# Optimization experiments

Hardware: AMD Instinct MI355X
Metric: run time of the kernel (lower is better)

Reference implementation:

```python
import jax, jax.numpy as jnp
import numpy as np
import math

B, S, D, H = 4, 1024, 1024, 16
DK = D // H
WINDOW = 128
NEG = -100000.0


def setup_inputs() -> dict:
    key = jax.random.key(0)
    kx, kw1, kb1, kw2, kb2 = jax.random.split(key, 5)
    x = jax.random.normal(kx, (B, S, D), dtype=jnp.float32)
    # sliding-window band mask: True where |i-j| <= WINDOW
    i = jnp.arange(S)
    band = (jnp.abs(i[:, None] - i[None, :]) <= WINDOW)
    mask = jnp.broadcast_to(band, (B, S, S))
    # second structured mask: causal
    causal = (i[:, None] >= i[None, :])
    mask2 = jnp.broadcast_to(causal, (B, S, S))
    scale = 1.0 / math.sqrt(D)
    Wqkv = jax.random.normal(kw1, (D, 3 * D), dtype=jnp.float32) * scale
    bqkv = jax.random.normal(kb1, (3 * D,), dtype=jnp.float32) * 0.01
    Wo = jax.random.normal(kw2, (D, D), dtype=jnp.float32) * scale
    bo = jax.random.normal(kb2, (D,), dtype=jnp.float32) * 0.01
    return {"x": x, "mask": mask, "mask2": mask2, "Wqkv": Wqkv, "bqkv": bqkv, "Wo": Wo, "bo": bo}


def reference(x, mask, mask2, Wqkv, bqkv, Wo, bo):
    b, s, d = x.shape
    qkv = x @ Wqkv + bqkv                      # [b, s, 3d]
    q, k, v = jnp.split(qkv, 3, axis=-1)
    # [b, s, h, dk] -> [b, h, s, dk]
    q = q.reshape(b, s, H, DK).transpose(0, 2, 1, 3)
    k = k.reshape(b, s, H, DK).transpose(0, 2, 1, 3)
    v = v.reshape(b, s, H, DK).transpose(0, 2, 1, 3)
    scores = jnp.einsum('bhtd,bhsd->bhts', q, k) / math.sqrt(DK)
    scores = jnp.where(mask[:, None, :, :], scores, NEG)
    scores = jnp.where(mask2[:, None, :, :], scores, NEG)
    weights = jax.nn.softmax(scores, axis=-1)  # [b, h, t, s]
    context = jnp.einsum('bhts,bhsd->bhtd', weights, v)
    context = context.transpose(0, 2, 1, 3).reshape(b, s, d)
    context = context @ Wo + bo
    return (context, weights)
```

## Files before the change

### kernel.cpp

```cpp
#include <hip/hip_runtime.h>

typedef short bf16x8 __attribute__((ext_vector_type(8)));
typedef float floatx4 __attribute__((ext_vector_type(4)));

#define GLOBAL_AS __attribute__((address_space(1)))
#define LDS_AS __attribute__((address_space(3)))

__device__ __forceinline__ void gload_lds16(const ushort* g, ushort* l) {
  __builtin_amdgcn_global_load_lds((const GLOBAL_AS void*)g, (LDS_AS void*)l, 16, 0, 0);
}

__device__ __forceinline__ ushort f2bf(float x) {
  uint u = __float_as_uint(x);
  return (ushort)((u + 0x7fffu + ((u >> 16) & 1u)) >> 16);
}

__global__ __launch_bounds__(256) void k_f32_to_bf16(const float4* __restrict__ in,
                                                     ushort4* __restrict__ out, int n4) {
  int g = blockIdx.x * 256 + threadIdx.x;
  if (g < n4) {
    float4 v = in[g];
    ushort4 o;
    o.x = f2bf(v.x); o.y = f2bf(v.y); o.z = f2bf(v.z); o.w = f2bf(v.w);
    out[g] = o;
  }
}

__global__ __launch_bounds__(256) void k_transpose2(const float* __restrict__ W1,
                                                    ushort* __restrict__ O1,
                                                    const float* __restrict__ W2,
                                                    ushort* __restrict__ O2) {
  __shared__ float tile[32][33];
  int bx = blockIdx.x;
  const float* in; ushort* out; int N;
  if (bx < 96) { in = W1; out = O1; N = 3072; }
  else         { in = W2; out = O2; N = 1024; bx -= 96; }
  const int K = 1024;
  int n0 = bx * 32, k0 = blockIdx.y * 32;
  int tx = threadIdx.x & 31, ty = threadIdx.x >> 5;
  #pragma unroll
  for (int r = ty; r < 32; r += 8)
    tile[r][tx] = in[(size_t)(k0 + r) * N + n0 + tx];
  __syncthreads();
  #pragma unroll
  for (int r = ty; r < 32; r += 8)
    out[(size_t)(n0 + r) * K + k0 + tx] = f2bf(tile[tx][r]);
}

template <int OUT_BF16, int BN>
__global__ __launch_bounds__(256) void k_gemm_bt(const ushort* __restrict__ A,
                                                 const ushort* __restrict__ Bt,
                                                 const float* __restrict__ bias,
                                                 void* __restrict__ Cout,
                                                 int M, int N, int K) {
  constexpr int NI = BN / 32;
  constexpr int NB = BN / 64;
  __shared__ ushort As[128 * 32];
  __shared__ ushort Bs[BN * 32];
  const int t = threadIdx.x;
  const int m0 = blockIdx.y * 128, n0 = blockIdx.x * BN;
  const int w = t >> 6, l = t & 63;
  const int wm = (w & 1) * 64, wn = (w >> 1) * (BN / 2);
  const int lr = l & 15, q8 = (l >> 4) * 8;
  const int lrow = l >> 2, lcol = (l & 3) * 8;

  floatx4 acc[4][NI];
  #pragma unroll
  for (int i = 0; i < 4; ++i)
    #pragma unroll
    for (int j = 0; j < NI; ++j) acc[i][j] = (floatx4){0.f, 0.f, 0.f, 0.f};

  for (int k0 = 0; k0 < K; k0 += 32) {
    __syncthreads();
    #pragma unroll
    for (int i = 0; i < 2; ++i) {
      int r0 = (w * 2 + i) * 16;
      gload_lds16(A + (size_t)(m0 + r0 + lrow) * K + k0 + lcol, As + r0 * 32);
    }
    #pragma unroll
    for (int i = 0; i < NB; ++i) {
      int r0 = (w * NB + i) * 16;
      gload_lds16(Bt + (size_t)(n0 + r0 + lrow) * K + k0 + lcol, Bs + r0 * 32);
    }
    __syncthreads();
    bf16x8 af[4], bfr[NI];
    #pragma unroll
    for (int mi = 0; mi < 4; ++mi)
      af[mi] = *(const bf16x8*)(As + (wm + mi * 16 + lr) * 32 + q8);
    #pragma unroll
    for (int ni = 0; ni < NI; ++ni)
      bfr[ni] = *(const bf16x8*)(Bs + (wn + ni * 16 + lr) * 32 + q8);
    #pragma unroll
    for (int mi = 0; mi < 4; ++mi)
      #pragma unroll
      for (int ni = 0; ni < NI; ++ni)
        acc[mi][ni] = __builtin_amdgcn_mfma_f32_16x16x32_bf16(af[mi], bfr[ni], acc[mi][ni], 0, 0, 0);
  }

  const int rq = (l >> 4) * 4;
  #pragma unroll
  for (int ni = 0; ni < NI; ++ni) {
    int col = n0 + wn + ni * 16 + lr;
    float bv = bias[col];
    #pragma unroll
    for (int mi = 0; mi < 4; ++mi) {
      int row = m0 + wm + mi * 16 + rq;
      #pragma unroll
      for (int r2 = 0; r2 < 4; ++r2) {
        float v = acc[mi][ni][r2] + bv;
        size_t idx = (size_t)(row + r2) * N + col;
        if (OUT_BF16) ((ushort*)Cout)[idx] = f2bf(v);
        else          ((float*)Cout)[idx] = v;
      }
    }
  }
}

__global__ __launch_bounds__(256) void k_attn(const ushort* __restrict__ qkv,
                                              float* __restrict__ wout,
                                              ushort* __restrict__ ctxout) {
  __shared__ ushort smKP[192 * 68];
  __shared__ ushort smVT[64 * 200];
  __shared__ float smInv[64];

  const int t = threadIdx.x;
  const int w = t >> 6, l = t & 63;
  const int lr = l & 15, q8 = (l >> 4) * 8, q4 = (l >> 4) * 4;
  const int iblk = blockIdx.x & 15;
  const int h = (blockIdx.x >> 4) & 15;
  const int b = blockIdx.x >> 8;
  const int i0 = iblk * 64;
  const int jb0 = i0 - 128;
  const int tok0 = b * 1024 + i0;
  const int qoff = h * 64, koff = 1024 + h * 64, voff = 2048 + h * 64;
  const size_t wbase = ((size_t)(b * 16 + h) * 1024 + i0) * 1024;

  #pragma unroll
  for (int c = 0; c < 6; ++c) {
    int idx = t + 256 * c, row = idx >> 3, ch = idx & 7;
    int jsrc = jb0 + row; if (jsrc < 0) jsrc = 0;
    *(uint4*)(smKP + row * 68 + ch * 8) =
        *(const uint4*)(qkv + (size_t)(b * 1024 + jsrc) * 3072 + koff + ch * 8);
  }
  #pragma unroll
  for (int c = 0; c < 6; ++c) {
    int idx = t + 256 * c;
    int j = (idx & 15) + 16 * (idx >> 7);
    int d0 = ((idx >> 4) & 7) * 8;
    int jsrc = jb0 + j; if (jsrc < 0) jsrc = 0;
    uint4 u = *(const uint4*)(qkv + (size_t)(b * 1024 + jsrc) * 3072 + voff + d0);
    ushort* p = smVT + j;
    p[(d0 + 0) * 200] = (ushort)(u.x & 0xffffu);
    p[(d0 + 1) * 200] = (ushort)(u.x >> 16);
    p[(d0 + 2) * 200] = (ushort)(u.y & 0xffffu);
    p[(d0 + 3) * 200] = (ushort)(u.y >> 16);
    p[(d0 + 4) * 200] = (ushort)(u.z & 0xffffu);
    p[(d0 + 5) * 200] = (ushort)(u.z >> 16);
    p[(d0 + 6) * 200] = (ushort)(u.w & 0xffffu);
    p[(d0 + 7) * 200] = (ushort)(u.w >> 16);
  }

  const ushort* qrow = qkv + (size_t)(tok0 + w * 16 + lr) * 3072 + qoff;
  bf16x8 aq0 = *(const bf16x8*)(qrow + q8);
  bf16x8 aq1 = *(const bf16x8*)(qrow + 32 + q8);
  __syncthreads();

  floatx4 sc[12];
  #pragma unroll
  for (int ni = 0; ni < 12; ++ni) sc[ni] = (floatx4){0.f, 0.f, 0.f, 0.f};
  #pragma unroll
  for (int ni = 0; ni < 12; ++ni) {
    bf16x8 bk0 = *(const bf16x8*)(smKP + (ni * 16 + lr) * 68 + q8);
    bf16x8 bk1 = *(const bf16x8*)(smKP + (ni * 16 + lr) * 68 + 32 + q8);
    sc[ni] = __builtin_amdgcn_mfma_f32_16x16x32_bf16(aq0, bk0, sc[ni], 0, 0, 0);
    sc[ni] = __builtin_amdgcn_mfma_f32_16x16x32_bf16(aq1, bk1, sc[ni], 0, 0, 0);
  }
  __syncthreads();

  float mrow[4] = {-3e38f, -3e38f, -3e38f, -3e38f};
  #pragma unroll
  for (int ni = 0; ni < 12; ++ni) {
    int nj = ni * 16 + lr;
    #pragma unroll
    for (int reg = 0; reg < 4; ++reg) {
      int di = w * 16 + q4 + reg;
      bool valid = (nj >= di) & (nj <= di + 128) & (jb0 + nj >= 0);
      float s = valid ? sc[ni][reg] * 0.125f : -3e38f;
      sc[ni][reg] = s;
      mrow[reg] = fmaxf(mrow[reg], s);
    }
  }
  #pragma unroll
  for (int reg = 0; reg < 4; ++reg) {
    #pragma unroll
    for (int off = 1; off < 16; off <<= 1)
      mrow[reg] = fmaxf(mrow[reg], __shfl_xor(mrow[reg], off, 64));
  }
  float lrow[4] = {0.f, 0.f, 0.f, 0.f};
  #pragma unroll
  for (int ni = 0; ni < 12; ++ni) {
    #pragma unroll
    for (int reg = 0; reg < 4; ++reg) {
      float e = __expf(sc[ni][reg] - mrow[reg]);
      sc[ni][reg] = e;
      lrow[reg] += e;
    }
  }
  float inv[4];
  #pragma unroll
  for (int reg = 0; reg < 4; ++reg) {
    float s = lrow[reg];
    #pragma unroll
    for (int off = 1; off < 16; off <<= 1) s += __shfl_xor(s, off, 64);
    inv[reg] = 1.0f / s;
  }

  ushort* smP = smKP;
  #pragma unroll
  for (int ni = 0; ni < 12; ++ni) {
    int nj = ni * 16 + lr;
    #pragma unroll
    for (int reg = 0; reg < 4; ++reg) {
      int il = w * 16 + q4 + reg;
      smP[il * 204 + nj] = f2bf(sc[ni][reg]);
    }
  }
  if (lr == 0) {
    #pragma unroll
    for (int reg = 0; reg < 4; ++reg) smInv[w * 16 + q4 + reg] = inv[reg];
  }

  floatx4 oc[4];
  #pragma unroll
  for (int ni = 0; ni < 4; ++ni) oc[ni] = (floatx4){0.f, 0.f, 0.f, 0.f};
  #pragma unroll
  for (int ks = 0; ks < 6; ++ks) {
    bf16x8 ap = *(const bf16x8*)(smP + (w * 16 + lr) * 204 + ks * 32 + q8);
    #pragma unroll
    for (int ni = 0; ni < 4; ++ni) {
      bf16x8 bv = *(const bf16x8*)(smVT + (ni * 16 + lr) * 200 + ks * 32 + q8);
      oc[ni] = __builtin_amdgcn_mfma_f32_16x16x32_bf16(ap, bv, oc[ni], 0, 0, 0);
    }
  }

  #pragma unroll
  for (int ni = 0; ni < 4; ++ni) {
    int d = ni * 16 + lr;
    #pragma unroll
    for (int reg = 0; reg < 4; ++reg) {
      int il = w * 16 + q4 + reg;
      ctxout[(size_t)(tok0 + il) * 1024 + qoff + d] = f2bf(oc[ni][reg] * inv[reg]);
    }
  }

  __syncthreads();

  {
    const int j4 = t * 4;
    const unsigned nj4 = (unsigned)(j4 - jb0);
    const bool inband = nj4 < 192u;
    const int njc = inband ? (int)nj4 : 0;
    const float bandf = inband ? 1.0f : 0.0f;
    float* wp = wout + wbase + j4;
    const ushort* pp = smP + njc;
    #pragma unroll 4
    for (int r = 0; r < 64; ++r) {
      ushort4 pv = *(const ushort4*)(pp + r * 204);
      float iv = smInv[r] * bandf;
      floatx4 o = { __uint_as_float((uint)pv.x << 16) * iv,
                    __uint_as_float((uint)pv.y << 16) * iv,
                    __uint_as_float((uint)pv.z << 16) * iv,
                    __uint_as_float((uint)pv.w << 16) * iv };
      __builtin_nontemporal_store(o, (floatx4*)(wp + (size_t)r * 1024));
    }
  }
}

extern "C" void kernel_launch(void* const* d_in, const int* in_sizes, int n_in,
                              void* d_out, int out_size, void* d_ws, size_t ws_size,
                              hipStream_t stream) {
  const float* x    = (const float*)d_in[0];
  const float* Wqkv = (const float*)d_in[3];
  const float* bqkv = (const float*)d_in[4];
  const float* Wo   = (const float*)d_in[5];
  const float* bo   = (const float*)d_in[6];

  float* out_ctx = (float*)d_out;
  float* out_w   = out_ctx + (size_t)4 * 1024 * 1024;

  char* ws = (char*)d_ws;
  ushort* qkv_bf = (ushort*)(ws);
  ushort* ctx_bf = (ushort*)(ws + 25165824);
  ushort* x_bf   = (ushort*)(ws + 33554432);
  ushort* WqkvT  = (ushort*)(ws + 41943040);
  ushort* WoT    = (ushort*)(ws + 48234496);

  k_f32_to_bf16<<<4096, 256, 0, stream>>>((const float4*)x, (ushort4*)x_bf, 1048576);
  k_transpose2<<<dim3(128, 32), 256, 0, stream>>>(Wqkv, WqkvT, Wo, WoT);
  k_gemm_bt<1, 128><<<dim3(24, 32), 256, 0, stream>>>(x_bf, WqkvT, bqkv, qkv_bf, 4096, 3072, 1024);
  k_attn<<<1024, 256, 0, stream>>>(qkv_bf, out_w, ctx_bf);
  k_gemm_bt<0, 64><<<dim3(16, 32), 256, 0, stream>>>(ctx_bf, WoT, bo, out_ctx, 4096, 1024, 1024);
}
```

Baseline: 399.3 us.

## Merge prep kernels, load K via direct-to-LDS swizzle, reorder PV after weights store

Combines the x-to-bf16 conversion and the weight transposes into one launch, removing a kernel launch. K tiles are now loaded with global_load_lds into an XOR-swizzled unpadded LDS layout instead of going through registers, and the score reads apply the matching swizzle. The PV matmul and context store are moved after the large weights write, so the nontemporal store of the weights output can start earlier. Risks include swizzle bank-conflict behavior and more register pressure from keeping inv live longer.

```diff
diff --git a/kernel.cpp b/kernel.cpp
--- a/kernel.cpp
+++ b/kernel.cpp
@@ -15,28 +15,26 @@
   return (ushort)((u + 0x7fffu + ((u >> 16) & 1u)) >> 16);
 }
 
-__global__ __launch_bounds__(256) void k_f32_to_bf16(const float4* __restrict__ in,
-                                                     ushort4* __restrict__ out, int n4) {
-  int g = blockIdx.x * 256 + threadIdx.x;
-  if (g < n4) {
-    float4 v = in[g];
+__global__ __launch_bounds__(256) void k_prep(const float4* __restrict__ x, ushort4* __restrict__ xbf,
+                                              const float* __restrict__ W1, ushort* __restrict__ O1,
+                                              const float* __restrict__ W2, ushort* __restrict__ O2) {
+  int bx = blockIdx.x;
+  if (bx < 4096) {
+    int g = bx * 256 + threadIdx.x;
+    float4 v = x[g];
     ushort4 o;
     o.x = f2bf(v.x); o.y = f2bf(v.y); o.z = f2bf(v.z); o.w = f2bf(v.w);
-    out[g] = o;
-  }
-}
-
-__global__ __launch_bounds__(256) void k_transpose2(const float* __restrict__ W1,
-                                                    ushort* __restrict__ O1,
-                                                    const float* __restrict__ W2,
-                                                    ushort* __restrict__ O2) {
+    xbf[g] = o;
+    return;
+  }
   __shared__ float tile[32][33];
-  int bx = blockIdx.x;
+  int tb = bx - 4096;
+  int by = tb >> 7, bxx = tb & 127;
   const float* in; ushort* out; int N;
-  if (bx < 96) { in = W1; out = O1; N = 3072; }
-  else         { in = W2; out = O2; N = 1024; bx -= 96; }
+  if (bxx < 96) { in = W1; out = O1; N = 3072; }
+  else          { in = W2; out = O2; N = 1024; bxx -= 96; }
   const int K = 1024;
-  int n0 = bx * 32, k0 = blockIdx.y * 32;
+  int n0 = bxx * 32, k0 = by * 32;
   int tx = threadIdx.x & 31, ty = threadIdx.x >> 5;
   #pragma unroll
   for (int r = ty; r < 32; r += 8)
@@ -135,12 +133,14 @@
   const int qoff = h * 64, koff = 1024 + h * 64, voff = 2048 + h * 64;
   const size_t wbase = ((size_t)(b * 16 + h) * 1024 + i0) * 1024;
 
-  #pragma unroll
-  for (int c = 0; c < 6; ++c) {
-    int idx = t + 256 * c, row = idx >> 3, ch = idx & 7;
-    int jsrc = jb0 + row; if (jsrc < 0) jsrc = 0;
-    *(uint4*)(smKP + row * 68 + ch * 8) =
-        *(const uint4*)(qkv + (size_t)(b * 1024 + jsrc) * 3072 + koff + ch * 8);
+  {
+    int scol = ((l & 7) ^ (l >> 3)) * 8;
+    #pragma unroll
+    for (int c = 0; c < 6; ++c) {
+      int r0 = (c * 4 + w) * 8;
+      int jsrc = jb0 + r0 + (l >> 3); if (jsrc < 0) jsrc = 0;
+      gload_lds16(qkv + (size_t)(b * 1024 + jsrc) * 3072 + koff + scol, smKP + r0 * 64);
+    }
   }
   #pragma unroll
   for (int c = 0; c < 6; ++c) {
@@ -165,13 +165,15 @@
   bf16x8 aq1 = *(const bf16x8*)(qrow + 32 + q8);
   __syncthreads();
 
+  const int kc0 = q8 ^ ((lr & 7) << 3);
+  const int kc1 = (q8 + 32) ^ ((lr & 7) << 3);
   floatx4 sc[12];
   #pragma unroll
   for (int ni = 0; ni < 12; ++ni) sc[ni] = (floatx4){0.f, 0.f, 0.f, 0.f};
   #pragma unroll
   for (int ni = 0; ni < 12; ++ni) {
-    bf16x8 bk0 = *(const bf16x8*)(smKP + (ni * 16 + lr) * 68 + q8);
-    bf16x8 bk1 = *(const bf16x8*)(smKP + (ni * 16 + lr) * 68 + 32 + q8);
+    bf16x8 bk0 = *(const bf16x8*)(smKP + (ni * 16 + lr) * 64 + kc0);
+    bf16x8 bk1 = *(const bf16x8*)(smKP + (ni * 16 + lr) * 64 + kc1);
     sc[ni] = __builtin_amdgcn_mfma_f32_16x16x32_bf16(aq0, bk0, sc[ni], 0, 0, 0);
     sc[ni] = __builtin_amdgcn_mfma_f32_16x16x32_bf16(aq1, bk1, sc[ni], 0, 0, 0);
   }
@@ -229,30 +231,6 @@
     #pragma unroll
     for (int reg = 0; reg < 4; ++reg) smInv[w * 16 + q4 + reg] = inv[reg];
   }
-
-  floatx4 oc[4];
-  #pragma unroll
-  for (int ni = 0; ni < 4; ++ni) oc[ni] = (floatx4){0.f, 0.f, 0.f, 0.f};
-  #pragma unroll
-  for (int ks = 0; ks < 6; ++ks) {
-    bf16x8 ap = *(const bf16x8*)(smP + (w * 16 + lr) * 204 + ks * 32 + q8);
-    #pragma unroll
-    for (int ni = 0; ni < 4; ++ni) {
-      bf16x8 bv = *(const bf16x8*)(smVT + (ni * 16 + lr) * 200 + ks * 32 + q8);
-      oc[ni] = __builtin_amdgcn_mfma_f32_16x16x32_bf16(ap, bv, oc[ni], 0, 0, 0);
-    }
-  }
-
-  #pragma unroll
-  for (int ni = 0; ni < 4; ++ni) {
-    int d = ni * 16 + lr;
-    #pragma unroll
-    for (int reg = 0; reg < 4; ++reg) {
-      int il = w * 16 + q4 + reg;
-      ctxout[(size_t)(tok0 + il) * 1024 + qoff + d] = f2bf(oc[ni][reg] * inv[reg]);
-    }
-  }
-
   __syncthreads();
 
   {
@@ -274,6 +252,29 @@
       __builtin_nontemporal_store(o, (floatx4*)(wp + (size_t)r * 1024));
     }
   }
+
+  floatx4 oc[4];
+  #pragma unroll
+  for (int ni = 0; ni < 4; ++ni) oc[ni] = (floatx4){0.f, 0.f, 0.f, 0.f};
+  #pragma unroll
+  for (int ks = 0; ks < 6; ++ks) {
+    bf16x8 ap = *(const bf16x8*)(smP + (w * 16 + lr) * 204 + ks * 32 + q8);
+    #pragma unroll
+    for (int ni = 0; ni < 4; ++ni) {
+      bf16x8 bv = *(const bf16x8*)(smVT + (ni * 16 + lr) * 200 + ks * 32 + q8);
+      oc[ni] = __builtin_amdgcn_mfma_f32_16x16x32_bf16(ap, bv, oc[ni], 0, 0, 0);
+    }
+  }
+
+  #pragma unroll
+  for (int ni = 0; ni < 4; ++ni) {
+    int d = ni * 16 + lr;
+    #pragma unroll
+    for (int reg = 0; reg < 4; ++reg) {
+      int il = w * 16 + q4 + reg;
+      ctxout[(size_t)(tok0 + il) * 1024 + qoff + d] = f2bf(oc[ni][reg] * inv[reg]);
+    }
+  }
 }
 
 extern "C" void kernel_launch(void* const* d_in, const int* in_sizes, int n_in,
@@ -295,8 +296,7 @@
   ushort* WqkvT  = (ushort*)(ws + 41943040);
   ushort* WoT    = (ushort*)(ws + 48234496);
 
-  k_f32_to_bf16<<<4096, 256, 0, stream>>>((const float4*)x, (ushort4*)x_bf, 1048576);
-  k_transpose2<<<dim3(128, 32), 256, 0, stream>>>(Wqkv, WqkvT, Wo, WoT);
+  k_prep<<<8192, 256, 0, stream>>>((const float4*)x, (ushort4*)x_bf, Wqkv, WqkvT, Wo, WoT);
   k_gemm_bt<1, 128><<<dim3(24, 32), 256, 0, stream>>>(x_bf, WqkvT, bqkv, qkv_bf, 4096, 3072, 1024);
   k_attn<<<1024, 256, 0, stream>>>(qkv_bf, out_w, ctx_bf);
   k_gemm_bt<0, 64><<<dim3(16, 32), 256, 0, stream>>>(ctx_bf, WoT, bo, out_ctx, 4096, 1024, 1024);
```

Measured after the change: 397.1 us. Within noise of the previous version (-0.6%).
